# Kernel optimization log

Measured on AMD Instinct MI355X. Metric: run time of the kernel, lower is better.

## Reference

```python
import jax, jax.numpy as jnp
import numpy as np

NUM_CONTEXT = 8  # context panels; +1 choice -> 9 panels, 72 ordered pairs (i != j)

_PAIRS = np.array([(i, j) for i in range(9) for j in range(9) if i != j], dtype=np.int32)
I_IDX = jnp.asarray(_PAIRS[:, 0])  # [72]
J_IDX = jnp.asarray(_PAIRS[:, 1])  # [72]


def setup_inputs() -> dict:
    key = jax.random.key(0)
    ks = jax.random.split(key, 10)
    B, C, F, H = 256, 8, 512, 256
    s_in = 1.0 / np.sqrt(2 * F)
    s_h = 1.0 / np.sqrt(H)
    return {
        "context_features": jax.random.normal(ks[0], (B, NUM_CONTEXT, F), jnp.float32),
        "choice_features": jax.random.normal(ks[1], (B, C, F), jnp.float32),
        "W1": jax.random.uniform(ks[2], (2 * F, H), jnp.float32, -s_in, s_in),
        "b1": jax.random.uniform(ks[3], (H,), jnp.float32, -s_in, s_in),
        "W2": jax.random.uniform(ks[4], (H, H), jnp.float32, -s_h, s_h),
        "b2": jax.random.uniform(ks[5], (H,), jnp.float32, -s_h, s_h),
        "W3": jax.random.uniform(ks[6], (H, H), jnp.float32, -s_h, s_h),
        "b3": jax.random.uniform(ks[7], (H,), jnp.float32, -s_h, s_h),
        "W4": jax.random.uniform(ks[8], (H, 1), jnp.float32, -s_h, s_h),
        "b4": jax.random.uniform(ks[9], (1,), jnp.float32, -s_h, s_h),
    }


def reference(context_features, choice_features, W1, b1, W2, b2, W3, b3, W4, b4):
    B, C, F = choice_features.shape[0], choice_features.shape[1], choice_features.shape[2]
    # panels[b, c, p, f]: 8 context panels + 1 choice panel per candidate choice
    ctx = jnp.broadcast_to(context_features[:, None, :, :], (B, C, NUM_CONTEXT, F))
    panels = jnp.concatenate([ctx, choice_features[:, :, None, :]], axis=2)  # [B,C,9,F]
    # all 72 ordered pairs (i != j), concatenated features -> [B,C,72,2F]
    pair = jnp.concatenate([panels[:, :, I_IDX, :], panels[:, :, J_IDX, :]], axis=-1)
    # g_theta MLP
    h = jax.nn.relu(pair @ W1 + b1)
    h = jax.nn.relu(h @ W2 + b2)        # [B,C,72,H]
    agg = h.mean(axis=2)                # [B,C,H]
    # f_phi MLP (dropout is identity in eval mode)
    g = jax.nn.relu(agg @ W3 + b3)
    score = g @ W4 + b4                 # [B,C,1]
    return score[..., 0]                # [B,C]
```

## Files before the change

### kernel.cpp

```cpp
#include <hip/hip_runtime.h>
#include <hip/hip_bf16.h>


typedef __bf16 bf16_t;
typedef bf16_t bf16x8 __attribute__((ext_vector_type(8)));
typedef bf16_t bf16x4 __attribute__((ext_vector_type(4)));
typedef float f32x4 __attribute__((ext_vector_type(4)));

#define MFMA16(a, b, c) __builtin_amdgcn_mfma_f32_16x16x32_bf16((a), (b), (c), 0, 0, 0)

__global__ __launch_bounds__(256) void prep_kernel(
    const float* __restrict__ W1, const float* __restrict__ W2,
    const float* __restrict__ W3, bf16_t* __restrict__ Wp,
    bf16_t* __restrict__ W2T, bf16_t* __restrict__ W3T) {
  const int idx = blockIdx.x * 256 + threadIdx.x;
  if (idx < 262144) {
    const int j = idx >> 9, k = idx & 511;
    const float v = (j < 256) ? W1[k * 256 + j] : W1[(512 + k) * 256 + (j - 256)];
    Wp[idx] = (bf16_t)v;
  } else if (idx < 327680) {
    const int s = idx - 262144;
    const int n = s >> 8, k = s & 255;
    W2T[s] = (bf16_t)W2[k * 256 + n];
  } else {
    const int s = idx - 327680;
    const int n = s >> 8, k = s & 255;
    W3T[s] = (bf16_t)W3[k * 256 + n];
  }
}

__global__ __launch_bounds__(256) void k1_kernel(
    const float* __restrict__ ctx, const float* __restrict__ cho,
    const bf16_t* __restrict__ Wp, bf16_t* __restrict__ UV) {
  __shared__ bf16_t As[64][264];
  const int bm = blockIdx.x & 63;
  const int bn = blockIdx.x >> 6;
  const int t = threadIdx.x;
  const int lane = t & 63;
  const int w = t >> 6;
  const int col = lane & 15;
  const int quad = lane >> 4;
  const int n = bn * 64 + w * 16 + col;
  const int sr = t >> 2;
  const int gr = bm * 64 + sr;
  const int bi = gr >> 4;
  const int p = gr & 15;
  const float* src = (p < 8) ? ctx + (size_t)(bi * 8 + p) * 512
                             : cho + (size_t)(bi * 8 + (p - 8)) * 512;
  const int cb = (t & 3) * 4;
  f32x4 acc[4] = {};
  for (int half = 0; half < 2; ++half) {
    const int kbase = half * 256;
    for (int i = 0; i < 16; ++i) {
      const int c = cb + i * 16;
      const f32x4 x = *(const f32x4*)(src + kbase + c);
      bf16x4 y;
      for (int e = 0; e < 4; ++e) y[e] = (bf16_t)x[e];
      *(bf16x4*)(&As[sr][c]) = y;
    }
    __syncthreads();
    for (int ks = 0; ks < 8; ++ks) {
      const int k = ks * 32 + quad * 8;
      bf16x8 af[4];
      for (int mt = 0; mt < 4; ++mt)
        af[mt] = *(const bf16x8*)(&As[mt * 16 + col][k]);
      const bf16x8 bf = *(const bf16x8*)(Wp + (size_t)n * 512 + kbase + k);
      for (int mt = 0; mt < 4; ++mt) acc[mt] = MFMA16(af[mt], bf, acc[mt]);
    }
    __syncthreads();
  }
  for (int mt = 0; mt < 4; ++mt)
    for (int reg = 0; reg < 4; ++reg) {
      const int r = bm * 64 + mt * 16 + quad * 4 + reg;
      UV[(size_t)r * 512 + n] = (bf16_t)acc[mt][reg];
    }
}

__global__ __launch_bounds__(512) void k2_kernel(
    const bf16_t* __restrict__ UV, const float* __restrict__ b1,
    const float* __restrict__ b2, const bf16_t* __restrict__ W2T,
    const bf16_t* __restrict__ W3T, const float* __restrict__ b3,
    const float* __restrict__ W4, const float* __restrict__ b4,
    float* __restrict__ out) {
  __shared__ char smem[52224];
  bf16_t (*h1)[136] = (bf16_t(*)[136])smem;
  float (*S)[256] = (float(*)[256])smem;
  bf16_t (*Ag)[264] = (bf16_t(*)[264])(smem + 9216);
  float (*red)[8] = (float(*)[8])(smem + 9216 + 8448);
  const int b = blockIdx.x;
  const int t = threadIdx.x;
  const int lane = t & 63;
  const int w = t >> 6;
  const int col = lane & 15;
  const int quad = lane >> 4;
  const bf16_t* su = nullptr;
  const bf16_t* sv = nullptr;
  int sr = 0, sc0 = 0;
  if (t < 384) {
    sr = t >> 1;
    sc0 = (t & 1) * 64;
    if (sr < 56) {
      const int i = sr / 7;
      const int jj = sr - i * 7;
      const int j = jj + (jj >= i ? 1 : 0);
      su = UV + (size_t)(b * 16 + i) * 512;
      sv = UV + (size_t)(b * 16 + j) * 512 + 256;
    } else if (sr >= 64) {
      const int ch = (sr - 64) >> 4;
      const int rr = (sr - 64) & 15;
      if (rr < 8) {
        su = UV + (size_t)(b * 16 + 8 + ch) * 512;
        sv = UV + (size_t)(b * 16 + rr) * 512 + 256;
      } else {
        su = UV + (size_t)(b * 16 + (rr - 8)) * 512;
        sv = UV + (size_t)(b * 16 + 8 + ch) * 512 + 256;
      }
    }
  }
  const int mtb = (w & 1) * 6;
  const int q = w >> 1;
  f32x4 acc[6][4] = {};
  for (int half = 0; half < 2; ++half) {
    const int kbase = half * 128;
    if (t < 384) {
      if (su) {
        for (int c = sc0; c < sc0 + 64; c += 8) {
          const bf16x8 u8 = *(const bf16x8*)(su + kbase + c);
          const bf16x8 v8 = *(const bf16x8*)(sv + kbase + c);
          const f32x4 bb0 = *(const f32x4*)(b1 + kbase + c);
          const f32x4 bb1 = *(const f32x4*)(b1 + kbase + c + 4);
          bf16x8 y;
          for (int e = 0; e < 4; ++e)
            y[e] = (bf16_t)fmaxf((float)u8[e] + (float)v8[e] + bb0[e], 0.0f);
          for (int e = 0; e < 4; ++e)
            y[4 + e] = (bf16_t)fmaxf((float)u8[4 + e] + (float)v8[4 + e] + bb1[e], 0.0f);
          *(bf16x8*)(&h1[sr][c]) = y;
        }
      } else {
        for (int c = sc0; c < sc0 + 64; c += 8)
          *(bf16x8*)(&h1[sr][c]) = (bf16x8)0.0f;
      }
    }
    __syncthreads();
    for (int ks = 0; ks < 4; ++ks) {
      const int k = ks * 32 + quad * 8;
      bf16x8 af[6], bf[4];
      for (int mt = 0; mt < 6; ++mt)
        af[mt] = *(const bf16x8*)(&h1[(mtb + mt) * 16 + col][k]);
      for (int nt = 0; nt < 4; ++nt) {
        const int n = q * 64 + nt * 16 + col;
        bf[nt] = *(const bf16x8*)(W2T + (size_t)n * 256 + kbase + k);
      }
      for (int mt = 0; mt < 6; ++mt)
        for (int nt = 0; nt < 4; ++nt)
          acc[mt][nt] = MFMA16(af[mt], bf[nt], acc[mt][nt]);
    }
    __syncthreads();
  }
  for (int nt = 0; nt < 4; ++nt) {
    const int n = q * 64 + nt * 16 + col;
    const float b2c = b2[n];
    float sctx = 0.0f;
    for (int mt = 0; mt < 6; ++mt) {
      const int gm = mtb + mt;
      float s = 0.0f;
      for (int reg = 0; reg < 4; ++reg) {
        const int row = gm * 16 + quad * 4 + reg;
        if (row < 56 || row >= 64) s += fmaxf(acc[mt][nt][reg] + b2c, 0.0f);
      }
      s += __shfl_xor(s, 16);
      s += __shfl_xor(s, 32);
      if (gm < 4) {
        sctx += s;
      } else if (lane < 16) {
        S[1 + (gm - 4)][n] = s;
      }
    }
    if (mtb == 0 && lane < 16) S[0][n] = sctx;
  }
  __syncthreads();
  {
    const int ch = t >> 6;
    const int n0 = (t & 63) * 4;
    bf16x4 y;
    for (int e = 0; e < 4; ++e)
      y[e] = (bf16_t)((S[0][n0 + e] + S[1 + ch][n0 + e]) * (1.0f / 72.0f));
    *(bf16x4*)(&Ag[ch][n0]) = y;
    *(bf16x4*)(&Ag[8 + ch][n0]) = (bf16x4)0.0f;
  }
  __syncthreads();
  f32x4 acc2[2] = {};
  for (int ks = 0; ks < 8; ++ks) {
    const int k = ks * 32 + quad * 8;
    const bf16x8 af = *(const bf16x8*)(&Ag[col][k]);
    for (int nt = 0; nt < 2; ++nt) {
      const int n = w * 32 + nt * 16 + col;
      const bf16x8 bf = *(const bf16x8*)(W3T + (size_t)n * 256 + k);
      acc2[nt] = MFMA16(af, bf, acc2[nt]);
    }
  }
  for (int reg = 0; reg < 4; ++reg) {
    float pr = 0.0f;
    for (int nt = 0; nt < 2; ++nt) {
      const int n = w * 32 + nt * 16 + col;
      pr += fmaxf(acc2[nt][reg] + b3[n], 0.0f) * W4[n];
    }
    pr += __shfl_xor(pr, 1);
    pr += __shfl_xor(pr, 2);
    pr += __shfl_xor(pr, 4);
    pr += __shfl_xor(pr, 8);
    if (col == 0 && quad < 2) red[w][quad * 4 + reg] = pr;
  }
  __syncthreads();
  if (t < 8) {
    float sc = b4[0];
    for (int ww = 0; ww < 8; ++ww) sc += red[ww][t];
    out[b * 8 + t] = sc;
  }
}

extern "C" void kernel_launch(void* const* d_in, const int* in_sizes, int n_in,
                              void* d_out, int out_size, void* d_ws, size_t ws_size,
                              hipStream_t stream) {
  (void)in_sizes; (void)n_in; (void)out_size; (void)ws_size;
  const float* ctx = (const float*)d_in[0];
  const float* cho = (const float*)d_in[1];
  const float* W1  = (const float*)d_in[2];
  const float* b1  = (const float*)d_in[3];
  const float* W2  = (const float*)d_in[4];
  const float* b2  = (const float*)d_in[5];
  const float* W3  = (const float*)d_in[6];
  const float* b3  = (const float*)d_in[7];
  const float* W4  = (const float*)d_in[8];
  const float* b4  = (const float*)d_in[9];
  char* ws = (char*)d_ws;
  bf16_t* Wp   = (bf16_t*)(ws + 0);
  bf16_t* W2T  = (bf16_t*)(ws + 524288);
  bf16_t* W3T  = (bf16_t*)(ws + 655360);
  bf16_t* UV   = (bf16_t*)(ws + 786432);
  float*  out  = (float*)d_out;

  prep_kernel<<<dim3(1536), dim3(256), 0, stream>>>(W1, W2, W3, Wp, W2T, W3T);
  k1_kernel<<<dim3(512), dim3(256), 0, stream>>>(ctx, cho, Wp, UV);
  k2_kernel<<<dim3(256), dim3(512), 0, stream>>>(UV, b1, b2, W2T, W3T, b3, W4, b4, out);
}
```

Baseline: 112.4 us.

## Tile weight transpose via shared memory and widen k1 blocks to 512 threads

The weight prep kernel now transposes 64x64 tiles through padded shared memory instead of using strided per-element reads, so both the global loads and the stores are coalesced. k1 uses 512-thread blocks that each cover 128 output columns, halving the grid and reusing each staged A tile across twice as many columns. k2 skips re-zeroing the padding rows of h1 on the second half, since they stay zero. The cost is fewer blocks in prep and k1, which gives less parallelism across the GPU.

```diff
diff --git a/kernel.cpp b/kernel.cpp
--- a/kernel.cpp
+++ b/kernel.cpp
@@ -13,23 +13,43 @@
     const float* __restrict__ W1, const float* __restrict__ W2,
     const float* __restrict__ W3, bf16_t* __restrict__ Wp,
     bf16_t* __restrict__ W2T, bf16_t* __restrict__ W3T) {
-  const int idx = blockIdx.x * 256 + threadIdx.x;
-  if (idx < 262144) {
-    const int j = idx >> 9, k = idx & 511;
-    const float v = (j < 256) ? W1[k * 256 + j] : W1[(512 + k) * 256 + (j - 256)];
-    Wp[idx] = (bf16_t)v;
-  } else if (idx < 327680) {
-    const int s = idx - 262144;
-    const int n = s >> 8, k = s & 255;
-    W2T[s] = (bf16_t)W2[k * 256 + n];
+  __shared__ float Ts[64][65];
+  const int b = blockIdx.x;
+  const int t = threadIdx.x;
+  const int r = t >> 6;
+  const int c = t & 63;
+  const float* srcP;
+  bf16_t* dstP;
+  int srcRow, srcCol, dr0, dc0, dstride;
+  if (b < 64) {
+    const int k0 = (b >> 3) * 64, j0 = (b & 7) * 64;
+    srcP = W1; dstP = Wp; dstride = 512;
+    srcRow = (j0 < 256) ? k0 : 512 + k0;
+    srcCol = (j0 < 256) ? j0 : j0 - 256;
+    dr0 = j0; dc0 = k0;
+  } else if (b < 80) {
+    const int s = b - 64;
+    const int k0 = (s >> 2) * 64, n0 = (s & 3) * 64;
+    srcP = W2; dstP = W2T; dstride = 256;
+    srcRow = k0; srcCol = n0; dr0 = n0; dc0 = k0;
   } else {
-    const int s = idx - 327680;
-    const int n = s >> 8, k = s & 255;
-    W3T[s] = (bf16_t)W3[k * 256 + n];
-  }
-}
-
-__global__ __launch_bounds__(256) void k1_kernel(
+    const int s = b - 80;
+    const int k0 = (s >> 2) * 64, n0 = (s & 3) * 64;
+    srcP = W3; dstP = W3T; dstride = 256;
+    srcRow = k0; srcCol = n0; dr0 = n0; dc0 = k0;
+  }
+  for (int i = 0; i < 16; ++i) {
+    const int a = i * 4 + r;
+    Ts[a][c] = srcP[(size_t)(srcRow + a) * 256 + srcCol + c];
+  }
+  __syncthreads();
+  for (int i = 0; i < 16; ++i) {
+    const int j = i * 4 + r;
+    dstP[(size_t)(dr0 + j) * dstride + dc0 + c] = (bf16_t)Ts[c][j];
+  }
+}
+
+__global__ __launch_bounds__(512) void k1_kernel(
     const float* __restrict__ ctx, const float* __restrict__ cho,
     const bf16_t* __restrict__ Wp, bf16_t* __restrict__ UV) {
   __shared__ bf16_t As[64][264];
@@ -40,19 +60,19 @@
   const int w = t >> 6;
   const int col = lane & 15;
   const int quad = lane >> 4;
-  const int n = bn * 64 + w * 16 + col;
-  const int sr = t >> 2;
+  const int n = bn * 128 + w * 16 + col;
+  const int sr = t >> 3;
   const int gr = bm * 64 + sr;
   const int bi = gr >> 4;
   const int p = gr & 15;
   const float* src = (p < 8) ? ctx + (size_t)(bi * 8 + p) * 512
                              : cho + (size_t)(bi * 8 + (p - 8)) * 512;
-  const int cb = (t & 3) * 4;
+  const int cb = (t & 7) * 4;
   f32x4 acc[4] = {};
   for (int half = 0; half < 2; ++half) {
     const int kbase = half * 256;
-    for (int i = 0; i < 16; ++i) {
-      const int c = cb + i * 16;
+    for (int i = 0; i < 8; ++i) {
+      const int c = cb + i * 32;
       const f32x4 x = *(const f32x4*)(src + kbase + c);
       bf16x4 y;
       for (int e = 0; e < 4; ++e) y[e] = (bf16_t)x[e];
@@ -136,7 +156,7 @@
             y[4 + e] = (bf16_t)fmaxf((float)u8[4 + e] + (float)v8[4 + e] + bb1[e], 0.0f);
           *(bf16x8*)(&h1[sr][c]) = y;
         }
-      } else {
+      } else if (half == 0) {
         for (int c = sc0; c < sc0 + 64; c += 8)
           *(bf16x8*)(&h1[sr][c]) = (bf16x8)0.0f;
       }
@@ -240,7 +260,7 @@
   bf16_t* UV   = (bf16_t*)(ws + 786432);
   float*  out  = (float*)d_out;
 
-  prep_kernel<<<dim3(1536), dim3(256), 0, stream>>>(W1, W2, W3, Wp, W2T, W3T);
-  k1_kernel<<<dim3(512), dim3(256), 0, stream>>>(ctx, cho, Wp, UV);
+  prep_kernel<<<dim3(96), dim3(256), 0, stream>>>(W1, W2, W3, Wp, W2T, W3T);
+  k1_kernel<<<dim3(256), dim3(512), 0, stream>>>(ctx, cho, Wp, UV);
   k2_kernel<<<dim3(256), dim3(512), 0, stream>>>(UV, b1, b2, W2T, W3T, b3, W4, b4, out);
 }
```

Result: faster. 109.0 us (-3.0%).
